# Kernel optimization log

Measured on AMD Instinct MI355X. Metric: run time of the kernel, lower is better.

## Reference

```python
import jax, jax.numpy as jnp
import numpy as np

N, CIN, COUT, E, NDIR = 65536, 128, 128, 589824, 9


def sel_conv(x, src, dst, sel, W, b):
    # x: [N, Cin]; W: [D, Cin, Cout]; edges j->i: out[i] += x[j] @ W[sel]
    n = x.shape[0]
    xs = x[src]  # [E, Cin] gather
    out = jnp.zeros((n, W.shape[2]), x.dtype)
    for d in range(W.shape[0]):  # fixed small direction count (9 or 1)
        m = (sel == d).astype(x.dtype)[:, None]
        agg = jax.ops.segment_sum(xs * m, dst, num_segments=n)  # [N, Cin]
        out = out + agg @ W[d]
    return out + b


def bn_eval(x, g, be, rm, rv, eps=1e-5):
    return (x - rm) * (g * jax.lax.rsqrt(rv + eps)) + be


def setup_inputs() -> dict:
    key = jax.random.key(0)
    ks = jax.random.split(key, 24)
    s = 0.05
    inp = {
        "x": jax.random.normal(ks[0], (N, CIN), jnp.float32),
        "edge_index": jax.random.randint(ks[1], (2, E), 0, N),
        "selections": jax.random.randint(ks[2], (E,), 0, NDIR),
        "W1": jax.random.normal(ks[3], (NDIR, CIN, COUT), jnp.float32) * s,
        "b1": jax.random.normal(ks[4], (COUT,), jnp.float32) * s,
        "g1": 1.0 + jax.random.normal(ks[5], (COUT,), jnp.float32) * s,
        "be1": jax.random.normal(ks[6], (COUT,), jnp.float32) * s,
        "rm1": jax.random.normal(ks[7], (COUT,), jnp.float32) * s,
        "rv1": 0.5 + jax.random.uniform(ks[8], (COUT,), jnp.float32),
        "W2": jax.random.normal(ks[9], (NDIR, COUT, COUT), jnp.float32) * s,
        "b2": jax.random.normal(ks[10], (COUT,), jnp.float32) * s,
        "g2": 1.0 + jax.random.normal(ks[11], (COUT,), jnp.float32) * s,
        "be2": jax.random.normal(ks[12], (COUT,), jnp.float32) * s,
        "rm2": jax.random.normal(ks[13], (COUT,), jnp.float32) * s,
        "rv2": 0.5 + jax.random.uniform(ks[14], (COUT,), jnp.float32),
        "W3": jax.random.normal(ks[15], (1, CIN, COUT), jnp.float32) * s,
        "b3": jax.random.normal(ks[16], (COUT,), jnp.float32) * s,
        "g3": 1.0 + jax.random.normal(ks[17], (COUT,), jnp.float32) * s,
        "be3": jax.random.normal(ks[18], (COUT,), jnp.float32) * s,
        "rm3": jax.random.normal(ks[19], (COUT,), jnp.float32) * s,
        "rv3": 0.5 + jax.random.uniform(ks[20], (COUT,), jnp.float32),
    }
    return inp


def reference(x, edge_index, selections, W1, b1, g1, be1, rm1, rv1,
              W2, b2, g2, be2, rm2, rv2, W3, b3, g3, be3, rm3, rv3):
    src, dst = edge_index[0], edge_index[1]
    # conv1: SelectionConv(3x3) + BN + ELU
    h = jax.nn.elu(bn_eval(sel_conv(x, src, dst, selections, W1, b1), g1, be1, rm1, rv1))
    # conv2: SelectionConv(3x3) + BN + ELU
    h = jax.nn.elu(bn_eval(sel_conv(h, src, dst, selections, W2, b2), g2, be2, rm2, rv2))
    # conv3: SelectionConv(1x1) shortcut (only selection-0 edges)
    sc = sel_conv(x, src, dst, selections, W3, b3)
    return jax.nn.elu(bn_eval(h + sc, g3, be3, rm3, rv3))
```

## Files before the change

kernel.cpp:

```cpp
#include <hip/hip_runtime.h>
#include <hip/hip_bf16.h>
#include <math.h>

#define N_NODES 65536
#define NDIR 9
#define NEDGE 589824
#define NBINS (N_NODES*NDIR)
#define TILE_M 32
#define SKEY_CAP 1024
#define APITCH 136

typedef __attribute__((ext_vector_type(8))) short short8;
typedef __attribute__((ext_vector_type(4))) float f32x4;

__device__ inline float bf2f(unsigned short u){ return __uint_as_float(((unsigned int)u)<<16); }
__device__ inline unsigned short f2bf(float f){
  unsigned int x = __float_as_uint(f);
  x += 0x7fff + ((x>>16)&1);
  return (unsigned short)(x>>16);
}
__device__ inline float elu1(float x){ return x>0.f ? x : expm1f(x); }

__device__ inline void acc8(f32x4& a0, f32x4& a1, short8 v){
  a0[0] += bf2f((unsigned short)v[0]); a0[1] += bf2f((unsigned short)v[1]);
  a0[2] += bf2f((unsigned short)v[2]); a0[3] += bf2f((unsigned short)v[3]);
  a1[0] += bf2f((unsigned short)v[4]); a1[1] += bf2f((unsigned short)v[5]);
  a1[2] += bf2f((unsigned short)v[6]); a1[3] += bf2f((unsigned short)v[7]);
}

__global__ void prep_all(const float* __restrict__ x, unsigned short* __restrict__ xb,
                         const float* __restrict__ W1, const float* __restrict__ W2,
                         const float* __restrict__ W3,
                         const float* __restrict__ b1, const float* __restrict__ g1,
                         const float* __restrict__ be1, const float* __restrict__ rm1,
                         const float* __restrict__ rv1,
                         const float* __restrict__ b2, const float* __restrict__ g2,
                         const float* __restrict__ be2, const float* __restrict__ rm2,
                         const float* __restrict__ rv2,
                         const float* __restrict__ b3, const float* __restrict__ g3,
                         const float* __restrict__ be3, const float* __restrict__ rm3,
                         const float* __restrict__ rv3,
                         unsigned short* __restrict__ Wt1, unsigned short* __restrict__ Wt2,
                         float* __restrict__ bias1, float* __restrict__ bias2,
                         float* __restrict__ bias3, float* __restrict__ s3v,
                         int* __restrict__ hist){
  const float eps = 1e-5f;
  int b = blockIdx.x, tid = threadIdx.x;
  if (b < 576){
    int4 z = {0,0,0,0};
    *(int4*)&hist[(b*256 + tid)*4] = z;
  } else if (b < 1792){
    int idx = (b - 576)*256 + tid;
    if (idx < 1280*128) {
      int n = idx >> 7, k = idx & 127;
      float v;
      if (n < 1152) { int d = n >> 7, c = n & 127;
        float s = g1[c]*rsqrtf(rv1[c]+eps); v = W1[(d*128 + k)*128 + c] * s; }
      else { int c = n - 1152;
        float s = g3[c]*rsqrtf(rv3[c]+eps); v = W3[k*128 + c] * s; }
      Wt1[idx] = f2bf(v);
    } else {
      int j = idx - 1280*128;
      int n = j >> 7, k = j & 127;
      int d = n >> 7, c = n & 127;
      float s = g2[c]*rsqrtf(rv2[c]+eps);
      Wt2[j] = f2bf(W2[(d*128 + k)*128 + c] * s);
    }
  } else if (b == 1792){
    if (tid < 128){
      int c = tid;
      float s1 = g1[c]*rsqrtf(rv1[c]+eps);
      bias1[c] = (b1[c]-rm1[c])*s1 + be1[c];
      float s2 = g2[c]*rsqrtf(rv2[c]+eps);
      bias2[c] = (b2[c]-rm2[c])*s2 + be2[c];
      float s3 = g3[c]*rsqrtf(rv3[c]+eps);
      bias3[c] = (b3[c]-rm3[c])*s3 + be3[c];
      s3v[c] = s3;
    }
  } else {
    int i = ((b - 1793)*256 + tid)*8;
    f32x4 f0 = *(const f32x4*)(x + i);
    f32x4 f1 = *(const f32x4*)(x + i + 4);
    short8 t;
    #pragma unroll
    for (int j = 0; j < 4; j++){ t[j] = (short)f2bf(f0[j]); t[4+j] = (short)f2bf(f1[j]); }
    *(short8*)(xb + i) = t;
  }
}

__global__ void hist_k(const int* __restrict__ dst, const int* __restrict__ sel,
                       int* __restrict__ hist){
  int e = blockIdx.x*256 + threadIdx.x;
  atomicAdd(&hist[dst[e]*9 + sel[e]], 1);
}

__global__ void scan1_k(const int* __restrict__ in, int* __restrict__ out, int* __restrict__ bsum){
  __shared__ int wsum[4];
  int t = threadIdx.x;
  int base = blockIdx.x*1024 + t*4;
  int4 v = *(const int4*)(in + base);
  int s = v.x + v.y + v.z + v.w;
  int lane = t & 63, w = t >> 6;
  int inc = s;
  #pragma unroll
  for (int o = 1; o < 64; o <<= 1){ int n = __shfl_up(inc, o); if (lane >= o) inc += n; }
  if (lane == 63) wsum[w] = inc;
  __syncthreads();
  int acc = 0;
  for (int i = 0; i < w; i++) acc += wsum[i];
  int ex = acc + inc - s;
  out[base] = ex; out[base+1] = ex + v.x; out[base+2] = ex + v.x + v.y; out[base+3] = ex + v.x + v.y + v.z;
  if (t == 255) bsum[blockIdx.x] = acc + inc;
}

__global__ void scan3_k(int* __restrict__ rs, const int* __restrict__ bsumx, int* __restrict__ cursor){
  int i = blockIdx.x*256 + threadIdx.x;
  int v = rs[i] + bsumx[i >> 10];
  rs[i] = v; cursor[i] = v;
  if (i == 0) rs[NBINS] = NEDGE;
}

__global__ void scatter_k(const int* __restrict__ src, const int* __restrict__ dst,
                          const int* __restrict__ sel,
                          int* __restrict__ cursor, int* __restrict__ sorted){
  int e = blockIdx.x*256 + threadIdx.x;
  int bin = dst[e]*9 + sel[e];
  int pos = atomicAdd(&cursor[bin], 1);
  sorted[pos] = src[e];
}

__device__ __forceinline__ void mfma_tile(f32x4 acc[2][2],
                                          const unsigned short* agg,
                                          const unsigned short* __restrict__ Wd,
                                          int w, int q, int r){
  #pragma unroll
  for (int kk = 0; kk < 4; kk++){
    const unsigned short* wp = Wd + (size_t)(w*32 + r)*128 + kk*32 + q*8;
    short8 b0 = *(const short8*)wp;
    short8 b1 = *(const short8*)(wp + 16*128);
    #pragma unroll
    for (int mt = 0; mt < 2; mt++){
      short8 av = *(const short8*)&agg[(mt*16 + r)*APITCH + kk*32 + q*8];
      acc[mt][0] = __builtin_amdgcn_mfma_f32_16x16x32_bf16(av, b0, acc[mt][0], 0, 0, 0);
      acc[mt][1] = __builtin_amdgcn_mfma_f32_16x16x32_bf16(av, b1, acc[mt][1], 0, 0, 0);
    }
  }
}

template<int IS_L2>
__global__ __launch_bounds__(256, 8) void layer_k(
    const unsigned short* __restrict__ H,
    const unsigned short* __restrict__ X,
    const unsigned short* __restrict__ Wf,
    const unsigned short* __restrict__ W3f,
    const int* __restrict__ rs, const int* __restrict__ sorted,
    const float* __restrict__ biasA, const float* __restrict__ bias3,
    const float* __restrict__ s3v,
    unsigned short* __restrict__ outB, float* __restrict__ outF){
  __shared__ __align__(16) unsigned short agg[TILE_M*APITCH];
  __shared__ int skey[SKEY_CAP];
  __shared__ int rsl[TILE_M*9 + 1];
  const int tid = threadIdx.x;
  const int w = tid >> 6, lane = tid & 63;
  const int q = lane >> 4, r = lane & 15;
  const int rid = tid >> 4, c = tid & 15;
  const int m0 = blockIdx.x * TILE_M;

  for (int i = tid; i <= TILE_M*9; i += 256) rsl[i] = rs[m0*9 + i];
  __syncthreads();
  const int lo = rsl[0];
  const int cnt = rsl[TILE_M*9] - lo;

  short8 pvA, pvB;
  {
    int aA = rsl[rid*9];
    int aB = rsl[(16+rid)*9];
    if (aA > NEDGE-1) aA = NEDGE-1;
    if (aB > NEDGE-1) aB = NEDGE-1;
    pvA = *(const short8*)(H + (size_t)sorted[aA]*128 + c*8);
    pvB = *(const short8*)(H + (size_t)sorted[aB]*128 + c*8);
  }

  for (int i = tid; i < cnt && i < SKEY_CAP; i += 256) skey[i] = sorted[lo + i];

  f32x4 acc[2][2];
  #pragma unroll
  for (int mt = 0; mt < 2; mt++){ acc[mt][0] = (f32x4){0,0,0,0}; acc[mt][1] = (f32x4){0,0,0,0}; }

  #pragma unroll 1
  for (int d = 0; d < 9; d++){
    __syncthreads();
    {
      int b = rid*9 + d;
      int s = rsl[b] - lo, e = rsl[b+1] - lo;
      f32x4 a0 = {0,0,0,0}, a1 = {0,0,0,0};
      if (e > s){
        acc8(a0, a1, pvA);
        for (int i = s+1; i < e; i++){
          int key = (i < SKEY_CAP) ? skey[i] : sorted[lo + i];
          short8 v = *(const short8*)(H + (size_t)key*128 + c*8);
          acc8(a0, a1, v);
        }
      }
      short8 o;
      o[0]=(short)f2bf(a0[0]); o[1]=(short)f2bf(a0[1]); o[2]=(short)f2bf(a0[2]); o[3]=(short)f2bf(a0[3]);
      o[4]=(short)f2bf(a1[0]); o[5]=(short)f2bf(a1[1]); o[6]=(short)f2bf(a1[2]); o[7]=(short)f2bf(a1[3]);
      *(short8*)&agg[rid*APITCH + c*8] = o;
    }
    {
      int b = (16 + rid)*9 + d;
      int s = rsl[b] - lo, e = rsl[b+1] - lo;
      f32x4 a0 = {0,0,0,0}, a1 = {0,0,0,0};
      if (e > s){
        acc8(a0, a1, pvB);
        for (int i = s+1; i < e; i++){
          int key = (i < SKEY_CAP) ? skey[i] : sorted[lo + i];
          short8 v = *(const short8*)(H + (size_t)key*128 + c*8);
          acc8(a0, a1, v);
        }
      }
      short8 o;
      o[0]=(short)f2bf(a0[0]); o[1]=(short)f2bf(a0[1]); o[2]=(short)f2bf(a0[2]); o[3]=(short)f2bf(a0[3]);
      o[4]=(short)f2bf(a1[0]); o[5]=(short)f2bf(a1[1]); o[6]=(short)f2bf(a1[2]); o[7]=(short)f2bf(a1[3]);
      *(short8*)&agg[(16 + rid)*APITCH + c*8] = o;
    }
    if (d < 8){
      int aA = rsl[rid*9 + d + 1];
      int aB = rsl[(16+rid)*9 + d + 1];
      if (aA > NEDGE-1) aA = NEDGE-1;
      if (aB > NEDGE-1) aB = NEDGE-1;
      pvA = *(const short8*)(H + (size_t)sorted[aA]*128 + c*8);
      pvB = *(const short8*)(H + (size_t)sorted[aB]*128 + c*8);
    } else if (IS_L2){
      int aA = rsl[rid*9];
      int aB = rsl[(16+rid)*9];
      if (aA > NEDGE-1) aA = NEDGE-1;
      if (aB > NEDGE-1) aB = NEDGE-1;
      pvA = *(const short8*)(X + (size_t)sorted[aA]*128 + c*8);
      pvB = *(const short8*)(X + (size_t)sorted[aB]*128 + c*8);
    }
    __syncthreads();
    mfma_tile(acc, agg, Wf + (size_t)d*128*128, w, q, r);
  }

  if constexpr (!IS_L2){
    #pragma unroll
    for (int mt = 0; mt < 2; mt++)
      #pragma unroll
      for (int n2 = 0; n2 < 2; n2++){
        int col = w*32 + n2*16 + r;
        float bA = biasA[col];
        #pragma unroll
        for (int rr = 0; rr < 4; rr++){
          int row = m0 + mt*16 + q*4 + rr;
          outB[(size_t)row*128 + col] = f2bf(elu1(acc[mt][n2][rr] + bA));
        }
      }
  } else {
    __syncthreads();
    {
      int b = rid*9;
      int s = rsl[b] - lo, e = rsl[b+1] - lo;
      f32x4 a0 = {0,0,0,0}, a1 = {0,0,0,0};
      if (e > s){
        acc8(a0, a1, pvA);
        for (int i = s+1; i < e; i++){
          int key = (i < SKEY_CAP) ? skey[i] : sorted[lo + i];
          short8 v = *(const short8*)(X + (size_t)key*128 + c*8);
          acc8(a0, a1, v);
        }
      }
      short8 o;
      o[0]=(short)f2bf(a0[0]); o[1]=(short)f2bf(a0[1]); o[2]=(short)f2bf(a0[2]); o[3]=(short)f2bf(a0[3]);
      o[4]=(short)f2bf(a1[0]); o[5]=(short)f2bf(a1[1]); o[6]=(short)f2bf(a1[2]); o[7]=(short)f2bf(a1[3]);
      *(short8*)&agg[rid*APITCH + c*8] = o;
    }
    {
      int b = (16 + rid)*9;
      int s = rsl[b] - lo, e = rsl[b+1] - lo;
      f32x4 a0 = {0,0,0,0}, a1 = {0,0,0,0};
      if (e > s){
        acc8(a0, a1, pvB);
        for (int i = s+1; i < e; i++){
          int key = (i < SKEY_CAP) ? skey[i] : sorted[lo + i];
          short8 v = *(const short8*)(X + (size_t)key*128 + c*8);
          acc8(a0, a1, v);
        }
      }
      short8 o;
      o[0]=(short)f2bf(a0[0]); o[1]=(short)f2bf(a0[1]); o[2]=(short)f2bf(a0[2]); o[3]=(short)f2bf(a0[3]);
      o[4]=(short)f2bf(a1[0]); o[5]=(short)f2bf(a1[1]); o[6]=(short)f2bf(a1[2]); o[7]=(short)f2bf(a1[3]);
      *(short8*)&agg[(16 + rid)*APITCH + c*8] = o;
    }
    __syncthreads();
    f32x4 sca[2][2];
    #pragma unroll
    for (int mt = 0; mt < 2; mt++){ sca[mt][0] = (f32x4){0,0,0,0}; sca[mt][1] = (f32x4){0,0,0,0}; }
    mfma_tile(sca, agg, W3f, w, q, r);
    #pragma unroll
    for (int mt = 0; mt < 2; mt++)
      #pragma unroll
      for (int n2 = 0; n2 < 2; n2++){
        int col = w*32 + n2*16 + r;
        float bA = biasA[col], b3 = bias3[col], s3 = s3v[col];
        #pragma unroll
        for (int rr = 0; rr < 4; rr++){
          int row = m0 + mt*16 + q*4 + rr;
          float h = elu1(acc[mt][n2][rr] + bA);
          outF[(size_t)row*128 + col] = elu1(h*s3 + sca[mt][n2][rr] + b3);
        }
      }
  }
}

extern "C" void kernel_launch(void* const* d_in, const int* in_sizes, int n_in,
                              void* d_out, int out_size, void* d_ws, size_t ws_size,
                              hipStream_t stream){
  const float* x   = (const float*)d_in[0];
  const int*   ei  = (const int*)d_in[1];
  const int*   sel = (const int*)d_in[2];
  const float* W1  = (const float*)d_in[3];
  const float* b1  = (const float*)d_in[4];
  const float* g1  = (const float*)d_in[5];
  const float* be1 = (const float*)d_in[6];
  const float* rm1 = (const float*)d_in[7];
  const float* rv1 = (const float*)d_in[8];
  const float* W2  = (const float*)d_in[9];
  const float* b2  = (const float*)d_in[10];
  const float* g2  = (const float*)d_in[11];
  const float* be2 = (const float*)d_in[12];
  const float* rm2 = (const float*)d_in[13];
  const float* rv2 = (const float*)d_in[14];
  const float* W3  = (const float*)d_in[15];
  const float* b3  = (const float*)d_in[16];
  const float* g3  = (const float*)d_in[17];
  const float* be3 = (const float*)d_in[18];
  const float* rm3 = (const float*)d_in[19];
  const float* rv3 = (const float*)d_in[20];

  char* ws = (char*)d_ws;
  unsigned short* xb   = (unsigned short*)(ws);
  unsigned short* h1   = (unsigned short*)(ws + 16777216);
  unsigned short* Wt1  = (unsigned short*)(ws + 33554432);
  unsigned short* Wt2  = (unsigned short*)(ws + 33882112);
  float* bias1  = (float*)(ws + 34177024);
  float* bias2  = bias1 + 128;
  float* bias3  = bias1 + 256;
  float* s3v    = bias1 + 384;
  int* hist     = (int*)(ws + 34179072);
  int* rs       = (int*)(ws + 36538368);
  int* cursor   = (int*)(ws + 38897920);
  int* bsum     = (int*)(ws + 41257216);
  int* bsumx    = (int*)(ws + 41261312);
  int* bsumT    = (int*)(ws + 41265408);
  int* sorted   = (int*)(ws + 41265664);

  const int* srcp = ei;
  const int* dstp = ei + NEDGE;

  prep_all<<<5889, 256, 0, stream>>>(x, xb, W1, W2, W3,
                                     b1, g1, be1, rm1, rv1,
                                     b2, g2, be2, rm2, rv2,
                                     b3, g3, be3, rm3, rv3,
                                     Wt1, Wt2, bias1, bias2, bias3, s3v, hist);
  hist_k<<<NEDGE/256, 256, 0, stream>>>(dstp, sel, hist);
  scan1_k<<<NBINS/1024, 256, 0, stream>>>(hist, rs, bsum);
  scan1_k<<<1, 256, 0, stream>>>(bsum, bsumx, bsumT);
  scan3_k<<<NBINS/256, 256, 0, stream>>>(rs, bsumx, cursor);
  scatter_k<<<NEDGE/256, 256, 0, stream>>>(srcp, dstp, sel, cursor, sorted);

  layer_k<0><<<2048, 256, 0, stream>>>(xb, nullptr, Wt1, nullptr, rs, sorted,
                                       bias1, nullptr, nullptr, h1, nullptr);
  layer_k<1><<<2048, 256, 0, stream>>>(h1, xb, Wt2, Wt1 + 1152*128, rs, sorted,
                                       bias2, bias3, s3v, nullptr, (float*)d_out);
}
```

Before: 371.4 us.

## Bucket edges by destination only and sub-sort by direction in shared memory

The global CSR build now uses one bin per destination node instead of per (node, direction), packing the direction into the upper bits of each sorted source index. This shrinks the histogram, scan and cursor arrays ninefold. Each layer block then runs its own shared-memory counting sort over its edge slice to rebuild per-direction ranges, with a fallback that scans global memory when a slice exceeds the cap. The cost is extra LDS atomics and block barriers in the layer kernels, and the removal of the next-row gather prefetch.

```diff
diff --git a/kernel.cpp b/kernel.cpp
--- a/kernel.cpp
+++ b/kernel.cpp
@@ -5,9 +5,8 @@
 #define N_NODES 65536
 #define NDIR 9
 #define NEDGE 589824
-#define NBINS (N_NODES*NDIR)
 #define TILE_M 32
-#define SKEY_CAP 1024
+#define CAP 512
 #define APITCH 136
 
 typedef __attribute__((ext_vector_type(8))) short short8;
@@ -46,11 +45,11 @@
                          int* __restrict__ hist){
   const float eps = 1e-5f;
   int b = blockIdx.x, tid = threadIdx.x;
-  if (b < 576){
+  if (b < 64){
     int4 z = {0,0,0,0};
     *(int4*)&hist[(b*256 + tid)*4] = z;
-  } else if (b < 1792){
-    int idx = (b - 576)*256 + tid;
+  } else if (b < 1280){
+    int idx = (b - 64)*256 + tid;
     if (idx < 1280*128) {
       int n = idx >> 7, k = idx & 127;
       float v;
@@ -66,7 +65,7 @@
       float s = g2[c]*rsqrtf(rv2[c]+eps);
       Wt2[j] = f2bf(W2[(d*128 + k)*128 + c] * s);
     }
-  } else if (b == 1792){
+  } else if (b == 1280){
     if (tid < 128){
       int c = tid;
       float s1 = g1[c]*rsqrtf(rv1[c]+eps);
@@ -78,7 +77,7 @@
       s3v[c] = s3;
     }
   } else {
-    int i = ((b - 1793)*256 + tid)*8;
+    int i = ((b - 1281)*256 + tid)*8;
     f32x4 f0 = *(const f32x4*)(x + i);
     f32x4 f1 = *(const f32x4*)(x + i + 4);
     short8 t;
@@ -88,10 +87,9 @@
   }
 }
 
-__global__ void hist_k(const int* __restrict__ dst, const int* __restrict__ sel,
-                       int* __restrict__ hist){
+__global__ void hist_k(const int* __restrict__ dst, int* __restrict__ hist){
   int e = blockIdx.x*256 + threadIdx.x;
-  atomicAdd(&hist[dst[e]*9 + sel[e]], 1);
+  atomicAdd(&hist[dst[e]], 1);
 }
 
 __global__ void scan1_k(const int* __restrict__ in, int* __restrict__ out, int* __restrict__ bsum){
@@ -117,16 +115,15 @@
   int i = blockIdx.x*256 + threadIdx.x;
   int v = rs[i] + bsumx[i >> 10];
   rs[i] = v; cursor[i] = v;
-  if (i == 0) rs[NBINS] = NEDGE;
+  if (i == 0) rs[N_NODES] = NEDGE;
 }
 
 __global__ void scatter_k(const int* __restrict__ src, const int* __restrict__ dst,
                           const int* __restrict__ sel,
                           int* __restrict__ cursor, int* __restrict__ sorted){
   int e = blockIdx.x*256 + threadIdx.x;
-  int bin = dst[e]*9 + sel[e];
-  int pos = atomicAdd(&cursor[bin], 1);
-  sorted[pos] = src[e];
+  int pos = atomicAdd(&cursor[dst[e]], 1);
+  sorted[pos] = src[e] | (sel[e] << 16);
 }
 
 __device__ __forceinline__ void mfma_tile(f32x4 acc[2][2],
@@ -158,30 +155,57 @@
     const float* __restrict__ s3v,
     unsigned short* __restrict__ outB, float* __restrict__ outF){
   __shared__ __align__(16) unsigned short agg[TILE_M*APITCH];
-  __shared__ int skey[SKEY_CAP];
-  __shared__ int rsl[TILE_M*9 + 1];
+  __shared__ int skey[CAP];
+  __shared__ unsigned short skey2[CAP];
+  __shared__ int rsl2[TILE_M + 1];
+  __shared__ int po[TILE_M*9];
+  __shared__ int wo[TILE_M*9];
   const int tid = threadIdx.x;
   const int w = tid >> 6, lane = tid & 63;
   const int q = lane >> 4, r = lane & 15;
   const int rid = tid >> 4, c = tid & 15;
   const int m0 = blockIdx.x * TILE_M;
 
-  for (int i = tid; i <= TILE_M*9; i += 256) rsl[i] = rs[m0*9 + i];
-  __syncthreads();
-  const int lo = rsl[0];
-  const int cnt = rsl[TILE_M*9] - lo;
-
-  short8 pvA, pvB;
+  if (tid <= TILE_M) rsl2[tid] = rs[m0 + tid];
+  for (int i = tid; i < TILE_M*9; i += 256) wo[i] = 0;
+  __syncthreads();
+  const int lo = rsl2[0];
+  const int cnt = rsl2[TILE_M] - lo;
+  for (int i = tid; i < cnt && i < CAP; i += 256) skey[i] = sorted[lo + i];
+  __syncthreads();
+
   {
-    int aA = rsl[rid*9];
-    int aB = rsl[(16+rid)*9];
-    if (aA > NEDGE-1) aA = NEDGE-1;
-    if (aB > NEDGE-1) aB = NEDGE-1;
-    pvA = *(const short8*)(H + (size_t)sorted[aA]*128 + c*8);
-    pvB = *(const short8*)(H + (size_t)sorted[aB]*128 + c*8);
-  }
-
-  for (int i = tid; i < cnt && i < SKEY_CAP; i += 256) skey[i] = sorted[lo + i];
+    const int nl8 = tid >> 3, sub = tid & 7;
+    int s = rsl2[nl8] - lo, e = rsl2[nl8+1] - lo;
+    if (e > CAP) e = CAP;
+    for (int i = s + sub; i < e; i += 8)
+      atomicAdd(&wo[nl8*9 + (skey[i] >> 16)], 1);
+  }
+  __syncthreads();
+  if (tid < TILE_M){
+    int base = rsl2[tid] - lo;
+    if (base > CAP) base = CAP;
+    #pragma unroll
+    for (int d = 0; d < 9; d++){
+      int b = tid*9 + d;
+      po[b] = base;
+      int cc = wo[b];
+      wo[b] = base;
+      base += cc;
+    }
+  }
+  __syncthreads();
+  {
+    const int nl8 = tid >> 3, sub = tid & 7;
+    int s = rsl2[nl8] - lo, e = rsl2[nl8+1] - lo;
+    if (e > CAP) e = CAP;
+    for (int i = s + sub; i < e; i += 8){
+      int k = skey[i];
+      int pos = atomicAdd(&wo[nl8*9 + (k >> 16)], 1);
+      skey2[pos] = (unsigned short)k;
+    }
+  }
+  __syncthreads();
 
   f32x4 acc[2][2];
   #pragma unroll
@@ -189,16 +213,22 @@
 
   #pragma unroll 1
   for (int d = 0; d < 9; d++){
-    __syncthreads();
+    if (d) __syncthreads();
     {
       int b = rid*9 + d;
-      int s = rsl[b] - lo, e = rsl[b+1] - lo;
+      int s = po[b], e = wo[b];
       f32x4 a0 = {0,0,0,0}, a1 = {0,0,0,0};
-      if (e > s){
-        acc8(a0, a1, pvA);
-        for (int i = s+1; i < e; i++){
-          int key = (i < SKEY_CAP) ? skey[i] : sorted[lo + i];
-          short8 v = *(const short8*)(H + (size_t)key*128 + c*8);
+      for (int i = s; i < e; i++){
+        int key = skey2[i];
+        short8 v = *(const short8*)(H + (size_t)key*128 + c*8);
+        acc8(a0, a1, v);
+      }
+      int ts = rsl2[rid] - lo; if (ts < CAP) ts = CAP;
+      int te = rsl2[rid+1] - lo;
+      for (int i = ts; i < te; i++){
+        int k = sorted[lo + i];
+        if ((k >> 16) == d){
+          short8 v = *(const short8*)(H + (size_t)(k & 0xFFFF)*128 + c*8);
           acc8(a0, a1, v);
         }
       }
@@ -209,13 +239,19 @@
     }
     {
       int b = (16 + rid)*9 + d;
-      int s = rsl[b] - lo, e = rsl[b+1] - lo;
+      int s = po[b], e = wo[b];
       f32x4 a0 = {0,0,0,0}, a1 = {0,0,0,0};
-      if (e > s){
-        acc8(a0, a1, pvB);
-        for (int i = s+1; i < e; i++){
-          int key = (i < SKEY_CAP) ? skey[i] : sorted[lo + i];
-          short8 v = *(const short8*)(H + (size_t)key*128 + c*8);
+      for (int i = s; i < e; i++){
+        int key = skey2[i];
+        short8 v = *(const short8*)(H + (size_t)key*128 + c*8);
+        acc8(a0, a1, v);
+      }
+      int ts = rsl2[16+rid] - lo; if (ts < CAP) ts = CAP;
+      int te = rsl2[16+rid+1] - lo;
+      for (int i = ts; i < te; i++){
+        int k = sorted[lo + i];
+        if ((k >> 16) == d){
+          short8 v = *(const short8*)(H + (size_t)(k & 0xFFFF)*128 + c*8);
           acc8(a0, a1, v);
         }
       }
@@ -223,21 +259,6 @@
       o[0]=(short)f2bf(a0[0]); o[1]=(short)f2bf(a0[1]); o[2]=(short)f2bf(a0[2]); o[3]=(short)f2bf(a0[3]);
       o[4]=(short)f2bf(a1[0]); o[5]=(short)f2bf(a1[1]); o[6]=(short)f2bf(a1[2]); o[7]=(short)f2bf(a1[3]);
       *(short8*)&agg[(16 + rid)*APITCH + c*8] = o;
-    }
-    if (d < 8){
-      int aA = rsl[rid*9 + d + 1];
-      int aB = rsl[(16+rid)*9 + d + 1];
-      if (aA > NEDGE-1) aA = NEDGE-1;
-      if (aB > NEDGE-1) aB = NEDGE-1;
-      pvA = *(const short8*)(H + (size_t)sorted[aA]*128 + c*8);
-      pvB = *(const short8*)(H + (size_t)sorted[aB]*128 + c*8);
-    } else if (IS_L2){
-      int aA = rsl[rid*9];
-      int aB = rsl[(16+rid)*9];
-      if (aA > NEDGE-1) aA = NEDGE-1;
-      if (aB > NEDGE-1) aB = NEDGE-1;
-      pvA = *(const short8*)(X + (size_t)sorted[aA]*128 + c*8);
-      pvB = *(const short8*)(X + (size_t)sorted[aB]*128 + c*8);
     }
     __syncthreads();
     mfma_tile(acc, agg, Wf + (size_t)d*128*128, w, q, r);
@@ -258,39 +279,30 @@
       }
   } else {
     __syncthreads();
-    {
-      int b = rid*9;
-      int s = rsl[b] - lo, e = rsl[b+1] - lo;
+    #pragma unroll
+    for (int t2 = 0; t2 < 2; t2++){
+      int nl = t2*16 + rid;
+      int b = nl*9;
+      int s = po[b], e = wo[b];
       f32x4 a0 = {0,0,0,0}, a1 = {0,0,0,0};
-      if (e > s){
-        acc8(a0, a1, pvA);
-        for (int i = s+1; i < e; i++){
-          int key = (i < SKEY_CAP) ? skey[i] : sorted[lo + i];
-          short8 v = *(const short8*)(X + (size_t)key*128 + c*8);
+      for (int i = s; i < e; i++){
+        int key = skey2[i];
+        short8 v = *(const short8*)(X + (size_t)key*128 + c*8);
+        acc8(a0, a1, v);
+      }
+      int ts = rsl2[nl] - lo; if (ts < CAP) ts = CAP;
+      int te = rsl2[nl+1] - lo;
+      for (int i = ts; i < te; i++){
+        int k = sorted[lo + i];
+        if ((k >> 16) == 0){
+          short8 v = *(const short8*)(X + (size_t)(k & 0xFFFF)*128 + c*8);
           acc8(a0, a1, v);
         }
       }
       short8 o;
       o[0]=(short)f2bf(a0[0]); o[1]=(short)f2bf(a0[1]); o[2]=(short)f2bf(a0[2]); o[3]=(short)f2bf(a0[3]);
       o[4]=(short)f2bf(a1[0]); o[5]=(short)f2bf(a1[1]); o[6]=(short)f2bf(a1[2]); o[7]=(short)f2bf(a1[3]);
-      *(short8*)&agg[rid*APITCH + c*8] = o;
-    }
-    {
-      int b = (16 + rid)*9;
-      int s = rsl[b] - lo, e = rsl[b+1] - lo;
-      f32x4 a0 = {0,0,0,0}, a1 = {0,0,0,0};
-      if (e > s){
-        acc8(a0, a1, pvB);
-        for (int i = s+1; i < e; i++){
-          int key = (i < SKEY_CAP) ? skey[i] : sorted[lo + i];
-          short8 v = *(const short8*)(X + (size_t)key*128 + c*8);
-          acc8(a0, a1, v);
-        }
-      }
-      short8 o;
-      o[0]=(short)f2bf(a0[0]); o[1]=(short)f2bf(a0[1]); o[2]=(short)f2bf(a0[2]); o[3]=(short)f2bf(a0[3]);
-      o[4]=(short)f2bf(a1[0]); o[5]=(short)f2bf(a1[1]); o[6]=(short)f2bf(a1[2]); o[7]=(short)f2bf(a1[3]);
-      *(short8*)&agg[(16 + rid)*APITCH + c*8] = o;
+      *(short8*)&agg[nl*APITCH + c*8] = o;
     }
     __syncthreads();
     f32x4 sca[2][2];
@@ -358,15 +370,15 @@
   const int* srcp = ei;
   const int* dstp = ei + NEDGE;
 
-  prep_all<<<5889, 256, 0, stream>>>(x, xb, W1, W2, W3,
+  prep_all<<<5377, 256, 0, stream>>>(x, xb, W1, W2, W3,
                                      b1, g1, be1, rm1, rv1,
                                      b2, g2, be2, rm2, rv2,
                                      b3, g3, be3, rm3, rv3,
                                      Wt1, Wt2, bias1, bias2, bias3, s3v, hist);
-  hist_k<<<NEDGE/256, 256, 0, stream>>>(dstp, sel, hist);
-  scan1_k<<<NBINS/1024, 256, 0, stream>>>(hist, rs, bsum);
+  hist_k<<<NEDGE/256, 256, 0, stream>>>(dstp, hist);
+  scan1_k<<<N_NODES/1024, 256, 0, stream>>>(hist, rs, bsum);
   scan1_k<<<1, 256, 0, stream>>>(bsum, bsumx, bsumT);
-  scan3_k<<<NBINS/256, 256, 0, stream>>>(rs, bsumx, cursor);
+  scan3_k<<<N_NODES/256, 256, 0, stream>>>(rs, bsumx, cursor);
   scatter_k<<<NEDGE/256, 256, 0, stream>>>(srcp, dstp, sel, cursor, sorted);
 
   layer_k<0><<<2048, 256, 0, stream>>>(xb, nullptr, Wt1, nullptr, rs, sorted,
```

Result: faster. 364.0 us (-2.0%).
